# Optimization experiments

Measured on AMD Instinct MI355X. Metric: run time of the kernel, lower is better.

Reference implementation:

```python
import jax, jax.numpy as jnp
import numpy as np

SMOOTH = 1.0


def setup_inputs() -> dict:
    key = jax.random.key(0)
    ks = jax.random.split(key, 6)
    T, B, Q, h, w = 6, 2, 50, 72, 72
    N, H, W = 8, 288, 288  # total trajectories (4 per sample), GT mask resolution
    return {
        "pred_masks_long": jax.random.normal(ks[0], (T, B, Q, h, w), jnp.float32),
        "pred_masks_short": jax.random.normal(ks[1], (T, B, Q, h, w), jnp.float32),
        "pred_is_referred_long": jax.random.normal(ks[2], (T, B, Q, 2), jnp.float32),
        "pred_is_referred_short": jax.random.normal(ks[3], (T, B, Q, 2), jnp.float32),
        "tgt_masks": jax.random.uniform(ks[4], (T, N, H, W), jnp.float32),
        "ref_indices": jax.random.randint(ks[5], (B,), 0, 4, jnp.int32),
    }


def _resize_masks(pm, H, W):
    # pm: [T, B, Q, h, w] -> bilinear (align_corners=False) upsample, flatten B*Q
    T, B, Q, h, w = pm.shape
    pm = pm.reshape(T, B * Q, h, w)
    return jax.image.resize(pm, (T, B * Q, H, W), method="bilinear")


def _dice_cost(pred, tgt):
    # pred: [T, P, H, W] logits; tgt: [T, N, H, W] -> cost [P, N]
    T, P, H, W = pred.shape
    N = tgt.shape[1]
    p = jax.nn.sigmoid(pred).reshape(T, P, H * W)
    g = tgt.reshape(T, N, H * W)
    num = 2.0 * jnp.einsum("tps,tns->tpn", p, g)  # fused pairwise reduction
    den = p.sum(-1)[:, :, None] + g.sum(-1)[:, None, :]
    return ((num + SMOOTH) / (den + SMOOTH)).mean(0)


def _conditioned_iou(pred_long, pred_short):
    # per-query coefficient, [P, 1]
    T, P = pred_long.shape[:2]
    pl = jax.nn.sigmoid(pred_long).reshape(T, P, -1)
    ps = jax.nn.sigmoid(pred_short).reshape(T, P, -1)
    pl = pl * (pl > 0.5)
    ps = ps * (ps > 0.5)
    num = (pl * ps).sum(-1)
    den = pl.sum(-1)
    return (((num + SMOOTH) / (den + SMOOTH)).mean(0))[:, None]


def _is_referred_cost(pred_is_referred, ref_global, T, N):
    # pred_is_referred: [T, B, Q, 2] -> cost [B*Q, N]
    p = jax.nn.softmax(pred_is_referred.reshape(T, -1, 2), axis=-1)
    tgt = jnp.tile(jnp.array([0.0, 1.0], jnp.float32), (T, N, 1))
    tgt = tgt.at[:, ref_global, :].set(jnp.array([1.0, 0.0], jnp.float32))
    return -jnp.einsum("tpc,tnc->pn", p, tgt) / T


def reference(pred_masks_long, pred_masks_short, pred_is_referred_long,
              pred_is_referred_short, tgt_masks, ref_indices):
    T, B, Q = pred_masks_long.shape[:3]
    N, H, W = tgt_masks.shape[1], tgt_masks.shape[2], tgt_masks.shape[3]
    traj_per_sample = N // B
    ref_global = ref_indices + jnp.arange(B, dtype=ref_indices.dtype) * traj_per_sample

    long_m = _resize_masks(pred_masks_long, H, W)   # [T, B*Q, H, W]
    short_m = _resize_masks(pred_masks_short, H, W)

    cost_is_referred = (_is_referred_cost(pred_is_referred_long, ref_global, T, N)
                        + _is_referred_cost(pred_is_referred_short, ref_global, T, N))
    cost_dice = -_dice_cost(long_m, tgt_masks) - _dice_cost(short_m, tgt_masks)
    cost_iou = -_conditioned_iou(long_m, short_m)  # [B*Q, 1] broadcasts over N

    C = 1.0 * cost_is_referred + 1.0 * cost_dice + 1.0 * cost_iou
    return C.reshape(B, Q, N)
```

## Files before the change

kernel.cpp:

```cpp
#include <hip/hip_runtime.h>
#include <hip/hip_bf16.h>


#define T_      6
#define P_      100
#define N_      8
#define HIN     72
#define SIN     (HIN*HIN)
#define HOUT    288
#define S_OUT   (HOUT*HOUT)
#define NQG     7
#define NCH     36
#define PART_F  320
#define WS2_OFF (T_*NQG*NCH*PART_F)
#define SUMG_OFF (WS2_OFF + T_*NQG*PART_F)
#define GCHUNK  8
#define NQUAD   (S_OUT/4)
#define WLDS    6144
#define NLOG2E  (-1.4426950408889634f)

typedef __attribute__((ext_vector_type(8))) short short8;
typedef __attribute__((ext_vector_type(4))) float f32x4;
typedef __attribute__((ext_vector_type(2))) float f32x2;

__device__ __forceinline__ unsigned cvt_pk_bf16(float lo, float hi) {
    unsigned r;
    asm("v_cvt_pk_bf16_f32 %0, %1, %2" : "=v"(r) : "v"(lo), "v"(hi));
    return r;
}

__device__ __forceinline__ f32x2 sigm2m(f32x2 m) {
    f32x2 e;
    e.x = __builtin_amdgcn_exp2f(m.x);
    e.y = __builtin_amdgcn_exp2f(m.y);
    f32x2 d = e + 1.0f;
    f32x2 r;
    r.x = __builtin_amdgcn_rcpf(d.x);
    r.y = __builtin_amdgcn_rcpf(d.y);
    return r;
}

#define WRED(x) { x += __shfl_down(x,32); x += __shfl_down(x,16); x += __shfl_down(x,8); \
                  x += __shfl_down(x,4);  x += __shfl_down(x,2);  x += __shfl_down(x,1); }

__global__ __launch_bounds__(256, 4) void mfma_partial(
    const float* __restrict__ predL, const float* __restrict__ predS,
    const float* __restrict__ tgt, float* __restrict__ ws)
{
    __shared__ __align__(16) char smem[4*WLDS + 512];
    float* iredN = (float*)(smem + 4*WLDS);
    float* iredD = (float*)(smem + 4*WLDS + 256);
    float (*cred)[64][8] = (float (*)[64][8])smem;

    const int blk = blockIdx.x;
    const int t   = blk / (NQG*NCH);
    const int rem = blk % (NQG*NCH);
    const int qg  = rem / NCH;
    const int ch  = rem % NCH;

    const int lane = threadIdx.x & 63;
    const int wv   = threadIdx.x >> 6;
    char* actL = smem + wv*WLDS;
    char* actS = actL + 2048;
    char* gpl  = actL + 4096;

    const int hi   = lane >> 4;
    const int cell = lane & 15;
    const float* __restrict__ pLb[4];
    const float* __restrict__ pSb[4];
#pragma unroll
    for (int r = 0; r < 4; r++) {
        const int qv = min(qg*16 + r*4 + hi, P_-1);
        pLb[r] = predL + ((size_t)t*P_ + qv)*SIN;
        pSb[r] = predS + ((size_t)t*P_ + qv)*SIN;
    }

    const int gn = lane >> 3, gf = lane & 7;
    const float4* __restrict__ gsrc = (const float4*)tgt + (size_t)(t*8 + gn)*NQUAD;
    const int gwoff = (gn*128 + 8*gf) ^ ((gn&7)<<4);

    if (lane < 16) {
        *(uint2*)(gpl + ((8*128 + 8*lane) ^ 0)) = make_uint2(0x3F803F80u, 0x3F803F80u);
#pragma unroll
        for (int col = 9; col < 16; col++)
            *(uint2*)(gpl + ((col*128 + 8*lane) ^ ((col&7)<<4))) = make_uint2(0u, 0u);
    }

    f32x4 accL = {0.f,0.f,0.f,0.f}, accS = {0.f,0.f,0.f,0.f};
    f32x2 iN2[4], iD2[4];
#pragma unroll
    for (int r = 0; r < 4; r++) { iN2[r] = (f32x2)(0.f); iD2[r] = (f32x2)(0.f); }
    const int arow = lane & 15, kg = lane >> 4;

    for (int it = 0; it < 9; it++) {
        const int px0 = ch*2304 + it*256 + wv*64;

        {
            const int f4b = px0 >> 2;
            float4 ga = gsrc[f4b + gf];
            float4 gb = gsrc[f4b + gf + 8];
            uint2 pa, pb;
            pa.x = cvt_pk_bf16(ga.x, ga.y); pa.y = cvt_pk_bf16(ga.z, ga.w);
            pb.x = cvt_pk_bf16(gb.x, gb.y); pb.y = cvt_pk_bf16(gb.z, gb.w);
            *(uint2*)(gpl + gwoff) = pa;
            *(uint2*)(gpl + (gwoff ^ 64)) = pb;
        }

        const unsigned p = px0 + 4*cell;
        const int row  = p / 288u;
        const int col4 = (p % 288u) >> 2;
        const int ry = row & 3, j = row >> 2;
        int y0 = (ry < 2) ? j-1 : j;
        int y1 = y0 + 1;
        y0 = max(y0, 0); y1 = min(y1, HIN-1);
        const float wt = 0.375f + 0.5f*(float)(ry>>1) - 0.25f*(float)(ry&1);
        const float wtm = wt * NLOG2E;
        const float wbm = (1.0f - wt) * NLOG2E;
        const int im1 = max(col4-1, 0), ip1 = min(col4+1, HIN-1);
        const int o0 = y0*HIN, o1 = y1*HIN;

        f32x2 tap[4][6];
#pragma unroll
        for (int r = 0; r < 4; r++) {
            const float* __restrict__ pLq = pLb[r];
            const float* __restrict__ pSq = pSb[r];
            tap[r][0].x = pLq[o0+im1];  tap[r][0].y = pSq[o0+im1];
            tap[r][1].x = pLq[o0+col4]; tap[r][1].y = pSq[o0+col4];
            tap[r][2].x = pLq[o0+ip1];  tap[r][2].y = pSq[o0+ip1];
            tap[r][3].x = pLq[o1+im1];  tap[r][3].y = pSq[o1+im1];
            tap[r][4].x = pLq[o1+col4]; tap[r][4].y = pSq[o1+col4];
            tap[r][5].x = pLq[o1+ip1];  tap[r][5].y = pSq[o1+ip1];
        }

#pragma unroll
        for (int r = 0; r < 4; r++) {
            f32x2 vm = tap[r][0]*wtm + tap[r][3]*wbm;
            f32x2 vc = tap[r][1]*wtm + tap[r][4]*wbm;
            f32x2 vp = tap[r][2]*wtm + tap[r][5]*wbm;
            f32x2 m0 = vm*0.375f + vc*0.625f;
            f32x2 m1 = vm*0.125f + vc*0.875f;
            f32x2 m2 = vc*0.875f + vp*0.125f;
            f32x2 m3 = vc*0.625f + vp*0.375f;

            f32x2 a0 = sigm2m(m0), a1 = sigm2m(m1), a2 = sigm2m(m2), a3 = sigm2m(m3);

            f32x2 pl01, ps01, pl23, ps23;
            pl01.x = (m0.x < 0.f) ? a0.x : 0.f;  pl01.y = (m1.x < 0.f) ? a1.x : 0.f;
            ps01.x = (m0.y < 0.f) ? a0.y : 0.f;  ps01.y = (m1.y < 0.f) ? a1.y : 0.f;
            pl23.x = (m2.x < 0.f) ? a2.x : 0.f;  pl23.y = (m3.x < 0.f) ? a3.x : 0.f;
            ps23.x = (m2.y < 0.f) ? a2.y : 0.f;  ps23.y = (m3.y < 0.f) ? a3.y : 0.f;
            iN2[r] = pl01*ps01 + iN2[r];
            iN2[r] = pl23*ps23 + iN2[r];
            iD2[r] = iD2[r] + pl01 + pl23;

            uint2 wl, wsv;
            wl.x  = cvt_pk_bf16(a0.x, a1.x); wl.y  = cvt_pk_bf16(a2.x, a3.x);
            wsv.x = cvt_pk_bf16(a0.y, a1.y); wsv.y = cvt_pk_bf16(a2.y, a3.y);
            const int qloc = r*4 + hi;
            const int aoff = (qloc*128 + 8*cell) ^ ((qloc&7)<<4);
            *(uint2*)(actL + aoff) = wl;
            *(uint2*)(actS + aoff) = wsv;
        }

#pragma unroll
        for (int ks = 0; ks < 2; ks++) {
            const int fo = (arow*128 + 64*ks + 16*kg) ^ ((arow&7)<<4);
            short8 fAL = *(const short8*)(actL + fo);
            short8 fAS = *(const short8*)(actS + fo);
            short8 fB  = *(const short8*)(gpl  + fo);
            accL = __builtin_amdgcn_mfma_f32_16x16x32_bf16(fAL, fB, accL, 0, 0, 0);
            accS = __builtin_amdgcn_mfma_f32_16x16x32_bf16(fAS, fB, accS, 0, 0, 0);
        }
    }

    float iN[4], iD[4];
#pragma unroll
    for (int r = 0; r < 4; r++) {
        iN[r] = iN2[r].x + iN2[r].y;
        iD[r] = iD2[r].x + iD2[r].y;
        iN[r] += __shfl_down(iN[r], 1); iN[r] += __shfl_down(iN[r], 2);
        iN[r] += __shfl_down(iN[r], 4); iN[r] += __shfl_down(iN[r], 8);
        iD[r] += __shfl_down(iD[r], 1); iD[r] += __shfl_down(iD[r], 2);
        iD[r] += __shfl_down(iD[r], 4); iD[r] += __shfl_down(iD[r], 8);
    }

    __syncthreads();
#pragma unroll
    for (int e = 0; e < 4; e++) { cred[wv][lane][e] = accL[e]; cred[wv][lane][4+e] = accS[e]; }
    if (cell == 0) {
#pragma unroll
        for (int r = 0; r < 4; r++) {
            iredN[wv*16 + r*4 + hi] = iN[r];
            iredD[wv*16 + r*4 + hi] = iD[r];
        }
    }
    __syncthreads();

    float* wsb = ws + (size_t)blk * PART_F;
    if (threadIdx.x < 64) {
        const int l = threadIdx.x;
        const int colx = l & 15, rb = (l >> 4) * 4;
        if (colx < 9) {
#pragma unroll
            for (int e = 0; e < 4; e++) {
                const float sLv = cred[0][l][e]+cred[1][l][e]+cred[2][l][e]+cred[3][l][e];
                const float sSv = cred[0][l][4+e]+cred[1][l][4+e]+cred[2][l][4+e]+cred[3][l][4+e];
                wsb[colx*16 + rb + e] = sLv;
                wsb[144 + colx*16 + rb + e] = sSv;
            }
        }
    }
    if (threadIdx.x < 16) {
        wsb[288 + threadIdx.x] = iredN[threadIdx.x] + iredN[16+threadIdx.x]
                               + iredN[32+threadIdx.x] + iredN[48+threadIdx.x];
        wsb[304 + threadIdx.x] = iredD[threadIdx.x] + iredD[16+threadIdx.x]
                               + iredD[32+threadIdx.x] + iredD[48+threadIdx.x];
    }
}

__global__ __launch_bounds__(256) void sumg_kernel(
    const float* __restrict__ tgt, float* __restrict__ ws)
{
    const int blk  = blockIdx.x;
    const int mask = blk / GCHUNK;
    const int c    = blk % GCHUNK;
    const float4* __restrict__ g = (const float4*)(tgt + (size_t)mask*S_OUT);
    const int per = NQUAD / GCHUNK;
    float s = 0.f;
    const int end = (c+1)*per;
    for (int idx = c*per + threadIdx.x; idx < end; idx += 256) {
        float4 v = g[idx];
        s += v.x + v.y + v.z + v.w;
    }
    WRED(s);
    __shared__ float r[4];
    if ((threadIdx.x & 63) == 0) r[threadIdx.x >> 6] = s;
    __syncthreads();
    if (threadIdx.x == 0) ws[SUMG_OFF + blk] = r[0]+r[1]+r[2]+r[3];
}

__global__ __launch_bounds__(320) void reduce_kernel(float* __restrict__ ws)
{
    const int tq = blockIdx.x;
    for (int s = threadIdx.x; s < PART_F; s += 320) {
        float acc = 0.f;
        const float* base = ws + (size_t)tq*NCH*PART_F + s;
#pragma unroll 4
        for (int c = 0; c < NCH; c++) acc += base[(size_t)c*PART_F];
        ws[WS2_OFF + (size_t)tq*PART_F + s] = acc;
    }
}

__global__ __launch_bounds__(64) void final_kernel(
    const float* __restrict__ pirL, const float* __restrict__ pirS,
    const int* __restrict__ refidx, const float* __restrict__ ws,
    float* __restrict__ out)
{
    const int gid = blockIdx.x*64 + threadIdx.x;
    if (gid >= P_*N_) return;
    const int p = gid >> 3, n = gid & 7;
    const int b = p / 50, qloc = p % 50;
    const int qg = p >> 4, row = p & 15;
    const int rg0 = refidx[0], rg1 = refidx[1] + 4;
    const bool isref = (n == rg0) || (n == rg1);

    float acc = 0.f;
    for (int t = 0; t < T_; t++) {
        const float* b2 = ws + WS2_OFF + (size_t)(t*NQG + qg)*PART_F;
        const float dL = b2[n*16 + row];
        const float sL = b2[128 + row];
        const float dS = b2[144 + n*16 + row];
        const float sS = b2[144 + 128 + row];
        const float iN = b2[288 + row];
        const float iD = b2[304 + row];
        float gS = 0.f;
#pragma unroll
        for (int c = 0; c < GCHUNK; c++) gS += ws[SUMG_OFF + (t*8+n)*GCHUNK + c];

        const float diceL = (2.f*dL + 1.f) / (sL + gS + 1.f);
        const float diceS = (2.f*dS + 1.f) / (sS + gS + 1.f);
        const float iou   = (iN + 1.f) / (iD + 1.f);
        const int ib = ((t*2 + b)*50 + qloc)*2;
        const float l0 = pirL[ib], l1 = pirL[ib+1];
        const float m0 = pirS[ib], m1 = pirS[ib+1];
        const float pl = isref ? 1.f/(1.f + __expf(l1 - l0)) : 1.f/(1.f + __expf(l0 - l1));
        const float ps = isref ? 1.f/(1.f + __expf(m1 - m0)) : 1.f/(1.f + __expf(m0 - m1));
        acc += diceL + diceS + iou + pl + ps;
    }
    out[gid] = -acc * (1.0f / (float)T_);
}

extern "C" void kernel_launch(void* const* d_in, const int* in_sizes, int n_in,
                              void* d_out, int out_size, void* d_ws, size_t ws_size,
                              hipStream_t stream) {
    const float* predL = (const float*)d_in[0];
    const float* predS = (const float*)d_in[1];
    const float* pirL  = (const float*)d_in[2];
    const float* pirS  = (const float*)d_in[3];
    const float* tgt   = (const float*)d_in[4];
    const int*   refix = (const int*)d_in[5];
    float* ws  = (float*)d_ws;
    float* out = (float*)d_out;

    mfma_partial<<<T_*NQG*NCH, 256, 0, stream>>>(predL, predS, tgt, ws);
    sumg_kernel<<<T_*N_*GCHUNK, 256, 0, stream>>>(tgt, ws);
    reduce_kernel<<<T_*NQG, 320, 0, stream>>>(ws);
    final_kernel<<<(P_*N_ + 63)/64, 64, 0, stream>>>(pirL, pirS, refix, ws, out);
}
```

Before: 66.92 us.

## Fold target-sum into MFMA via ones-padded rows; widen per-lane pixel work

Removes the separate sumg kernel by filling the unused padded query rows of the last query group with bf16 ones, so the MFMA product yields the per-target mask sums as a by-product that the final kernel reads. Each lane now processes 8 pixels for 2 query rows instead of 4 pixels for 4 rows, so the bilinear taps can share neighbouring loads and be fetched as float2, and the LDS activation stores become 16-byte writes. This trades one kernel launch and a full extra read of the targets for bf16-precision target sums and some extra register pressure.

New measurement: 85.07 us. 27.1% more time.

```diff
diff --git a/kernel.cpp b/kernel.cpp
--- a/kernel.cpp
+++ b/kernel.cpp
@@ -13,8 +13,6 @@
 #define NCH     36
 #define PART_F  320
 #define WS2_OFF (T_*NQG*NCH*PART_F)
-#define SUMG_OFF (WS2_OFF + T_*NQG*PART_F)
-#define GCHUNK  8
 #define NQUAD   (S_OUT/4)
 #define WLDS    6144
 #define NLOG2E  (-1.4426950408889634f)
@@ -40,9 +38,6 @@
     return r;
 }
 
-#define WRED(x) { x += __shfl_down(x,32); x += __shfl_down(x,16); x += __shfl_down(x,8); \
-                  x += __shfl_down(x,4);  x += __shfl_down(x,2);  x += __shfl_down(x,1); }
-
 __global__ __launch_bounds__(256, 4) void mfma_partial(
     const float* __restrict__ predL, const float* __restrict__ predS,
     const float* __restrict__ tgt, float* __restrict__ ws)
@@ -64,13 +59,16 @@
     char* actS = actL + 2048;
     char* gpl  = actL + 4096;
 
-    const int hi   = lane >> 4;
-    const int cell = lane & 15;
-    const float* __restrict__ pLb[4];
-    const float* __restrict__ pSb[4];
-#pragma unroll
-    for (int r = 0; r < 4; r++) {
-        const int qv = min(qg*16 + r*4 + hi, P_-1);
+    const int hi   = lane >> 3;
+    const int cell = lane & 7;
+    const float* __restrict__ pLb[2];
+    const float* __restrict__ pSb[2];
+    bool isPad[2];
+#pragma unroll
+    for (int r = 0; r < 2; r++) {
+        const int qglob = qg*16 + r*8 + hi;
+        isPad[r] = (qglob >= P_);
+        const int qv = min(qglob, P_-1);
         pLb[r] = predL + ((size_t)t*P_ + qv)*SIN;
         pSb[r] = predS + ((size_t)t*P_ + qv)*SIN;
     }
@@ -85,11 +83,20 @@
         for (int col = 9; col < 16; col++)
             *(uint2*)(gpl + ((col*128 + 8*lane) ^ ((col&7)<<4))) = make_uint2(0u, 0u);
     }
+    if (qg == NQG-1 && lane < 12) {
+        const int qloc = 4 + lane;
+#pragma unroll
+        for (int c8 = 0; c8 < 8; c8++) {
+            const int off = (qloc*128 + 16*c8) ^ ((qloc&7)<<4);
+            *(uint4*)(actL + off) = make_uint4(0x3F803F80u,0x3F803F80u,0x3F803F80u,0x3F803F80u);
+            *(uint4*)(actS + off) = make_uint4(0x3F803F80u,0x3F803F80u,0x3F803F80u,0x3F803F80u);
+        }
+    }
 
     f32x4 accL = {0.f,0.f,0.f,0.f}, accS = {0.f,0.f,0.f,0.f};
-    f32x2 iN2[4], iD2[4];
-#pragma unroll
-    for (int r = 0; r < 4; r++) { iN2[r] = (f32x2)(0.f); iD2[r] = (f32x2)(0.f); }
+    f32x2 iN2[2], iD2[2];
+#pragma unroll
+    for (int r = 0; r < 2; r++) { iN2[r] = (f32x2)(0.f); iD2[r] = (f32x2)(0.f); }
     const int arow = lane & 15, kg = lane >> 4;
 
     for (int it = 0; it < 9; it++) {
@@ -106,7 +113,7 @@
             *(uint2*)(gpl + (gwoff ^ 64)) = pb;
         }
 
-        const unsigned p = px0 + 4*cell;
+        const unsigned p = px0 + 8*cell;
         const int row  = p / 288u;
         const int col4 = (p % 288u) >> 2;
         const int ry = row & 3, j = row >> 2;
@@ -116,50 +123,66 @@
         const float wt = 0.375f + 0.5f*(float)(ry>>1) - 0.25f*(float)(ry&1);
         const float wtm = wt * NLOG2E;
         const float wbm = (1.0f - wt) * NLOG2E;
-        const int im1 = max(col4-1, 0), ip1 = min(col4+1, HIN-1);
+        const int cm = max(col4-1, 0), c2 = min(col4+2, HIN-1);
         const int o0 = y0*HIN, o1 = y1*HIN;
 
-        f32x2 tap[4][6];
-#pragma unroll
-        for (int r = 0; r < 4; r++) {
+#pragma unroll
+        for (int r = 0; r < 2; r++) {
             const float* __restrict__ pLq = pLb[r];
             const float* __restrict__ pSq = pSb[r];
-            tap[r][0].x = pLq[o0+im1];  tap[r][0].y = pSq[o0+im1];
-            tap[r][1].x = pLq[o0+col4]; tap[r][1].y = pSq[o0+col4];
-            tap[r][2].x = pLq[o0+ip1];  tap[r][2].y = pSq[o0+ip1];
-            tap[r][3].x = pLq[o1+im1];  tap[r][3].y = pSq[o1+im1];
-            tap[r][4].x = pLq[o1+col4]; tap[r][4].y = pSq[o1+col4];
-            tap[r][5].x = pLq[o1+ip1];  tap[r][5].y = pSq[o1+ip1];
-        }
-
-#pragma unroll
-        for (int r = 0; r < 4; r++) {
-            f32x2 vm = tap[r][0]*wtm + tap[r][3]*wbm;
-            f32x2 vc = tap[r][1]*wtm + tap[r][4]*wbm;
-            f32x2 vp = tap[r][2]*wtm + tap[r][5]*wbm;
-            f32x2 m0 = vm*0.375f + vc*0.625f;
-            f32x2 m1 = vm*0.125f + vc*0.875f;
-            f32x2 m2 = vc*0.875f + vp*0.125f;
-            f32x2 m3 = vc*0.625f + vp*0.375f;
+
+            const float2 tL01 = *(const float2*)(pLq + o0 + col4);
+            const float2 bL01 = *(const float2*)(pLq + o1 + col4);
+            const float2 tS01 = *(const float2*)(pSq + o0 + col4);
+            const float2 bS01 = *(const float2*)(pSq + o1 + col4);
+            const float tLm = pLq[o0+cm], tLp = pLq[o0+c2];
+            const float bLm = pLq[o1+cm], bLp = pLq[o1+c2];
+            const float tSm = pSq[o0+cm], tSp = pSq[o0+c2];
+            const float bSm = pSq[o1+cm], bSp = pSq[o1+c2];
+
+            f32x2 v0, v1, v2, v3;
+            v0.x = wtm*tLm    + wbm*bLm;    v0.y = wtm*tSm    + wbm*bSm;
+            v1.x = wtm*tL01.x + wbm*bL01.x; v1.y = wtm*tS01.x + wbm*bS01.x;
+            v2.x = wtm*tL01.y + wbm*bL01.y; v2.y = wtm*tS01.y + wbm*bS01.y;
+            v3.x = wtm*tLp    + wbm*bLp;    v3.y = wtm*tSp    + wbm*bSp;
+
+            f32x2 m0 = v0*0.375f + v1*0.625f;
+            f32x2 m1 = v0*0.125f + v1*0.875f;
+            f32x2 m2 = v1*0.875f + v2*0.125f;
+            f32x2 m3 = v1*0.625f + v2*0.375f;
+            f32x2 m4 = v1*0.375f + v2*0.625f;
+            f32x2 m5 = v1*0.125f + v2*0.875f;
+            f32x2 m6 = v2*0.875f + v3*0.125f;
+            f32x2 m7 = v2*0.625f + v3*0.375f;
 
             f32x2 a0 = sigm2m(m0), a1 = sigm2m(m1), a2 = sigm2m(m2), a3 = sigm2m(m3);
-
-            f32x2 pl01, ps01, pl23, ps23;
+            f32x2 a4 = sigm2m(m4), a5 = sigm2m(m5), a6 = sigm2m(m6), a7 = sigm2m(m7);
+
+            f32x2 pl01, ps01, pl23, ps23, pl45, ps45, pl67, ps67;
             pl01.x = (m0.x < 0.f) ? a0.x : 0.f;  pl01.y = (m1.x < 0.f) ? a1.x : 0.f;
             ps01.x = (m0.y < 0.f) ? a0.y : 0.f;  ps01.y = (m1.y < 0.f) ? a1.y : 0.f;
             pl23.x = (m2.x < 0.f) ? a2.x : 0.f;  pl23.y = (m3.x < 0.f) ? a3.x : 0.f;
             ps23.x = (m2.y < 0.f) ? a2.y : 0.f;  ps23.y = (m3.y < 0.f) ? a3.y : 0.f;
-            iN2[r] = pl01*ps01 + iN2[r];
-            iN2[r] = pl23*ps23 + iN2[r];
+            pl45.x = (m4.x < 0.f) ? a4.x : 0.f;  pl45.y = (m5.x < 0.f) ? a5.x : 0.f;
+            ps45.x = (m4.y < 0.f) ? a4.y : 0.f;  ps45.y = (m5.y < 0.f) ? a5.y : 0.f;
+            pl67.x = (m6.x < 0.f) ? a6.x : 0.f;  pl67.y = (m7.x < 0.f) ? a7.x : 0.f;
+            ps67.x = (m6.y < 0.f) ? a6.y : 0.f;  ps67.y = (m7.y < 0.f) ? a7.y : 0.f;
+            iN2[r] = pl01*ps01 + iN2[r];  iN2[r] = pl23*ps23 + iN2[r];
+            iN2[r] = pl45*ps45 + iN2[r];  iN2[r] = pl67*ps67 + iN2[r];
             iD2[r] = iD2[r] + pl01 + pl23;
-
-            uint2 wl, wsv;
-            wl.x  = cvt_pk_bf16(a0.x, a1.x); wl.y  = cvt_pk_bf16(a2.x, a3.x);
-            wsv.x = cvt_pk_bf16(a0.y, a1.y); wsv.y = cvt_pk_bf16(a2.y, a3.y);
-            const int qloc = r*4 + hi;
-            const int aoff = (qloc*128 + 8*cell) ^ ((qloc&7)<<4);
-            *(uint2*)(actL + aoff) = wl;
-            *(uint2*)(actS + aoff) = wsv;
+            iD2[r] = iD2[r] + pl45 + pl67;
+
+            if (!isPad[r]) {
+                uint4 wl4, ws4;
+                wl4.x = cvt_pk_bf16(a0.x, a1.x); wl4.y = cvt_pk_bf16(a2.x, a3.x);
+                wl4.z = cvt_pk_bf16(a4.x, a5.x); wl4.w = cvt_pk_bf16(a6.x, a7.x);
+                ws4.x = cvt_pk_bf16(a0.y, a1.y); ws4.y = cvt_pk_bf16(a2.y, a3.y);
+                ws4.z = cvt_pk_bf16(a4.y, a5.y); ws4.w = cvt_pk_bf16(a6.y, a7.y);
+                const int qloc = r*8 + hi;
+                const int aoff = (qloc*128 + 16*cell) ^ ((qloc&7)<<4);
+                *(uint4*)(actL + aoff) = wl4;
+                *(uint4*)(actS + aoff) = ws4;
+            }
         }
 
 #pragma unroll
@@ -173,15 +196,15 @@
         }
     }
 
-    float iN[4], iD[4];
-#pragma unroll
-    for (int r = 0; r < 4; r++) {
+    float iN[2], iD[2];
+#pragma unroll
+    for (int r = 0; r < 2; r++) {
         iN[r] = iN2[r].x + iN2[r].y;
         iD[r] = iD2[r].x + iD2[r].y;
-        iN[r] += __shfl_down(iN[r], 1); iN[r] += __shfl_down(iN[r], 2);
-        iN[r] += __shfl_down(iN[r], 4); iN[r] += __shfl_down(iN[r], 8);
-        iD[r] += __shfl_down(iD[r], 1); iD[r] += __shfl_down(iD[r], 2);
-        iD[r] += __shfl_down(iD[r], 4); iD[r] += __shfl_down(iD[r], 8);
+        iN[r] += __shfl_down(iN[r], 4); iN[r] += __shfl_down(iN[r], 2);
+        iN[r] += __shfl_down(iN[r], 1);
+        iD[r] += __shfl_down(iD[r], 4); iD[r] += __shfl_down(iD[r], 2);
+        iD[r] += __shfl_down(iD[r], 1);
     }
 
     __syncthreads();
@@ -189,9 +212,9 @@
     for (int e = 0; e < 4; e++) { cred[wv][lane][e] = accL[e]; cred[wv][lane][4+e] = accS[e]; }
     if (cell == 0) {
 #pragma unroll
-        for (int r = 0; r < 4; r++) {
-            iredN[wv*16 + r*4 + hi] = iN[r];
-            iredD[wv*16 + r*4 + hi] = iD[r];
+        for (int r = 0; r < 2; r++) {
+            iredN[wv*16 + r*8 + hi] = iN[r];
+            iredD[wv*16 + r*8 + hi] = iD[r];
         }
     }
     __syncthreads();
@@ -216,27 +239,6 @@
         wsb[304 + threadIdx.x] = iredD[threadIdx.x] + iredD[16+threadIdx.x]
                                + iredD[32+threadIdx.x] + iredD[48+threadIdx.x];
     }
-}
-
-__global__ __launch_bounds__(256) void sumg_kernel(
-    const float* __restrict__ tgt, float* __restrict__ ws)
-{
-    const int blk  = blockIdx.x;
-    const int mask = blk / GCHUNK;
-    const int c    = blk % GCHUNK;
-    const float4* __restrict__ g = (const float4*)(tgt + (size_t)mask*S_OUT);
-    const int per = NQUAD / GCHUNK;
-    float s = 0.f;
-    const int end = (c+1)*per;
-    for (int idx = c*per + threadIdx.x; idx < end; idx += 256) {
-        float4 v = g[idx];
-        s += v.x + v.y + v.z + v.w;
-    }
-    WRED(s);
-    __shared__ float r[4];
-    if ((threadIdx.x & 63) == 0) r[threadIdx.x >> 6] = s;
-    __syncthreads();
-    if (threadIdx.x == 0) ws[SUMG_OFF + blk] = r[0]+r[1]+r[2]+r[3];
 }
 
 __global__ __launch_bounds__(320) void reduce_kernel(float* __restrict__ ws)
@@ -273,9 +275,7 @@
         const float sS = b2[144 + 128 + row];
         const float iN = b2[288 + row];
         const float iD = b2[304 + row];
-        float gS = 0.f;
-#pragma unroll
-        for (int c = 0; c < GCHUNK; c++) gS += ws[SUMG_OFF + (t*8+n)*GCHUNK + c];
+        const float gS = ws[WS2_OFF + (size_t)(t*NQG + (NQG-1))*PART_F + n*16 + 4];
 
         const float diceL = (2.f*dL + 1.f) / (sL + gS + 1.f);
         const float diceS = (2.f*dS + 1.f) / (sS + gS + 1.f);
@@ -303,7 +303,6 @@
     float* out = (float*)d_out;
 
     mfma_partial<<<T_*NQG*NCH, 256, 0, stream>>>(predL, predS, tgt, ws);
-    sumg_kernel<<<T_*N_*GCHUNK, 256, 0, stream>>>(tgt, ws);
     reduce_kernel<<<T_*NQG, 320, 0, stream>>>(ws);
     final_kernel<<<(P_*N_ + 63)/64, 64, 0, stream>>>(pirL, pirS, refix, ws, out);
 }
```

## Fold target-mask sums into MFMA via padded ones rows, drop sumg kernel

Applied to the files above, without the earlier changes.

The last query group has 12 padding rows (queries 100-111). They are now filled with bf16 ones in the activation tiles, so the MFMA computes the per-target mask sums for free, and the final kernel reads gS from that slot. This removes the separate sumg kernel launch and its second pass over the target masks. The target loads are also hoisted ahead of the tap loads behind a sched_barrier to overlap latency. The trade-off is that gS is now a bf16-rounded sum rather than an fp32 one, which costs some precision.

Measured after the change: 60.66 us. 9.3% less time.

```diff
diff --git a/kernel.cpp b/kernel.cpp
--- a/kernel.cpp
+++ b/kernel.cpp
@@ -13,8 +13,6 @@
 #define NCH     36
 #define PART_F  320
 #define WS2_OFF (T_*NQG*NCH*PART_F)
-#define SUMG_OFF (WS2_OFF + T_*NQG*PART_F)
-#define GCHUNK  8
 #define NQUAD   (S_OUT/4)
 #define WLDS    6144
 #define NLOG2E  (-1.4426950408889634f)
@@ -40,9 +38,6 @@
     return r;
 }
 
-#define WRED(x) { x += __shfl_down(x,32); x += __shfl_down(x,16); x += __shfl_down(x,8); \
-                  x += __shfl_down(x,4);  x += __shfl_down(x,2);  x += __shfl_down(x,1); }
-
 __global__ __launch_bounds__(256, 4) void mfma_partial(
     const float* __restrict__ predL, const float* __restrict__ predS,
     const float* __restrict__ tgt, float* __restrict__ ws)
@@ -68,9 +63,12 @@
     const int cell = lane & 15;
     const float* __restrict__ pLb[4];
     const float* __restrict__ pSb[4];
+    bool isPad[4];
 #pragma unroll
     for (int r = 0; r < 4; r++) {
-        const int qv = min(qg*16 + r*4 + hi, P_-1);
+        const int qglob = qg*16 + r*4 + hi;
+        isPad[r] = (qglob >= P_);
+        const int qv = min(qglob, P_-1);
         pLb[r] = predL + ((size_t)t*P_ + qv)*SIN;
         pSb[r] = predS + ((size_t)t*P_ + qv)*SIN;
     }
@@ -85,6 +83,15 @@
         for (int col = 9; col < 16; col++)
             *(uint2*)(gpl + ((col*128 + 8*lane) ^ ((col&7)<<4))) = make_uint2(0u, 0u);
     }
+    if (qg == NQG-1 && lane < 12) {
+        const int qloc = 4 + lane;
+#pragma unroll
+        for (int c8 = 0; c8 < 8; c8++) {
+            const int off = (qloc*128 + 16*c8) ^ ((qloc&7)<<4);
+            *(uint4*)(actL + off) = make_uint4(0x3F803F80u,0x3F803F80u,0x3F803F80u,0x3F803F80u);
+            *(uint4*)(actS + off) = make_uint4(0x3F803F80u,0x3F803F80u,0x3F803F80u,0x3F803F80u);
+        }
+    }
 
     f32x4 accL = {0.f,0.f,0.f,0.f}, accS = {0.f,0.f,0.f,0.f};
     f32x2 iN2[4], iD2[4];
@@ -94,17 +101,6 @@
 
     for (int it = 0; it < 9; it++) {
         const int px0 = ch*2304 + it*256 + wv*64;
-
-        {
-            const int f4b = px0 >> 2;
-            float4 ga = gsrc[f4b + gf];
-            float4 gb = gsrc[f4b + gf + 8];
-            uint2 pa, pb;
-            pa.x = cvt_pk_bf16(ga.x, ga.y); pa.y = cvt_pk_bf16(ga.z, ga.w);
-            pb.x = cvt_pk_bf16(gb.x, gb.y); pb.y = cvt_pk_bf16(gb.z, gb.w);
-            *(uint2*)(gpl + gwoff) = pa;
-            *(uint2*)(gpl + (gwoff ^ 64)) = pb;
-        }
 
         const unsigned p = px0 + 4*cell;
         const int row  = p / 288u;
@@ -119,6 +115,10 @@
         const int im1 = max(col4-1, 0), ip1 = min(col4+1, HIN-1);
         const int o0 = y0*HIN, o1 = y1*HIN;
 
+        const int f4b = px0 >> 2;
+        float4 ga = gsrc[f4b + gf];
+        float4 gb = gsrc[f4b + gf + 8];
+
         f32x2 tap[4][6];
 #pragma unroll
         for (int r = 0; r < 4; r++) {
@@ -131,6 +131,15 @@
             tap[r][4].x = pLq[o1+col4]; tap[r][4].y = pSq[o1+col4];
             tap[r][5].x = pLq[o1+ip1];  tap[r][5].y = pSq[o1+ip1];
         }
+        __builtin_amdgcn_sched_barrier(0);
+
+        {
+            uint2 pa, pb;
+            pa.x = cvt_pk_bf16(ga.x, ga.y); pa.y = cvt_pk_bf16(ga.z, ga.w);
+            pb.x = cvt_pk_bf16(gb.x, gb.y); pb.y = cvt_pk_bf16(gb.z, gb.w);
+            *(uint2*)(gpl + gwoff) = pa;
+            *(uint2*)(gpl + (gwoff ^ 64)) = pb;
+        }
 
 #pragma unroll
         for (int r = 0; r < 4; r++) {
@@ -153,13 +162,15 @@
             iN2[r] = pl23*ps23 + iN2[r];
             iD2[r] = iD2[r] + pl01 + pl23;
 
-            uint2 wl, wsv;
-            wl.x  = cvt_pk_bf16(a0.x, a1.x); wl.y  = cvt_pk_bf16(a2.x, a3.x);
-            wsv.x = cvt_pk_bf16(a0.y, a1.y); wsv.y = cvt_pk_bf16(a2.y, a3.y);
-            const int qloc = r*4 + hi;
-            const int aoff = (qloc*128 + 8*cell) ^ ((qloc&7)<<4);
-            *(uint2*)(actL + aoff) = wl;
-            *(uint2*)(actS + aoff) = wsv;
+            if (!isPad[r]) {
+                uint2 wl, wsv;
+                wl.x  = cvt_pk_bf16(a0.x, a1.x); wl.y  = cvt_pk_bf16(a2.x, a3.x);
+                wsv.x = cvt_pk_bf16(a0.y, a1.y); wsv.y = cvt_pk_bf16(a2.y, a3.y);
+                const int qloc = r*4 + hi;
+                const int aoff = (qloc*128 + 8*cell) ^ ((qloc&7)<<4);
+                *(uint2*)(actL + aoff) = wl;
+                *(uint2*)(actS + aoff) = wsv;
+            }
         }
 
 #pragma unroll
@@ -216,27 +227,6 @@
         wsb[304 + threadIdx.x] = iredD[threadIdx.x] + iredD[16+threadIdx.x]
                                + iredD[32+threadIdx.x] + iredD[48+threadIdx.x];
     }
-}
-
-__global__ __launch_bounds__(256) void sumg_kernel(
-    const float* __restrict__ tgt, float* __restrict__ ws)
-{
-    const int blk  = blockIdx.x;
-    const int mask = blk / GCHUNK;
-    const int c    = blk % GCHUNK;
-    const float4* __restrict__ g = (const float4*)(tgt + (size_t)mask*S_OUT);
-    const int per = NQUAD / GCHUNK;
-    float s = 0.f;
-    const int end = (c+1)*per;
-    for (int idx = c*per + threadIdx.x; idx < end; idx += 256) {
-        float4 v = g[idx];
-        s += v.x + v.y + v.z + v.w;
-    }
-    WRED(s);
-    __shared__ float r[4];
-    if ((threadIdx.x & 63) == 0) r[threadIdx.x >> 6] = s;
-    __syncthreads();
-    if (threadIdx.x == 0) ws[SUMG_OFF + blk] = r[0]+r[1]+r[2]+r[3];
 }
 
 __global__ __launch_bounds__(320) void reduce_kernel(float* __restrict__ ws)
@@ -273,9 +263,7 @@
         const float sS = b2[144 + 128 + row];
         const float iN = b2[288 + row];
         const float iD = b2[304 + row];
-        float gS = 0.f;
-#pragma unroll
-        for (int c = 0; c < GCHUNK; c++) gS += ws[SUMG_OFF + (t*8+n)*GCHUNK + c];
+        const float gS = ws[WS2_OFF + (size_t)(t*NQG + (NQG-1))*PART_F + n*16 + 4];
 
         const float diceL = (2.f*dL + 1.f) / (sL + gS + 1.f);
         const float diceS = (2.f*dS + 1.f) / (sS + gS + 1.f);
@@ -303,7 +291,6 @@
     float* out = (float*)d_out;
 
     mfma_partial<<<T_*NQG*NCH, 256, 0, stream>>>(predL, predS, tgt, ws);
-    sumg_kernel<<<T_*N_*GCHUNK, 256, 0, stream>>>(tgt, ws);
     reduce_kernel<<<T_*NQG, 320, 0, stream>>>(ws);
     final_kernel<<<(P_*N_ + 63)/64, 64, 0, stream>>>(pirL, pirS, refix, ws, out);
 }
```
